# Kernel optimization log

Hardware: AMD Instinct MI355X
Metric: run time of the kernel (lower is better)

## Reference

```python
import jax, jax.numpy as jnp
import numpy as np

B, T, C, H = 4, 2048, 1024, 16
D = C // H


def setup_inputs() -> dict:
    key = jax.random.key(0)
    ks = jax.random.split(key, 6)
    s = 1.0 / np.sqrt(C)
    return {
        "x": jax.random.normal(ks[0], (B, T, C), dtype=jnp.float32),
        "attention_mask": jnp.ones((B, 1, T), dtype=jnp.int32),
        "Wq": jax.random.normal(ks[1], (C, C), dtype=jnp.float32) * s,
        "bq": jnp.zeros((C,), dtype=jnp.float32),
        "Wk": jax.random.normal(ks[2], (C, C), dtype=jnp.float32) * s,
        "bk": jnp.zeros((C,), dtype=jnp.float32),
        "Wv": jax.random.normal(ks[3], (C, C), dtype=jnp.float32) * s,
        "bv": jnp.zeros((C,), dtype=jnp.float32),
        "Wp": jax.random.normal(ks[4], (C, C), dtype=jnp.float32) * s,
        "bp": jnp.zeros((C,), dtype=jnp.float32),
    }


def reference(x, attention_mask, Wq, bq, Wk, bk, Wv, bv, Wp, bp):
    b, t, c = x.shape
    d = c // H
    # projections (torch Linear: x @ W^T + b)
    q = (x @ Wq.T + bq).reshape(b, t, H, d).transpose(0, 2, 1, 3)  # [B,H,T,D]
    k = (x @ Wk.T + bk).reshape(b, t, H, d).transpose(0, 2, 1, 3)
    v = (x @ Wv.T + bv).reshape(b, t, H, d).transpose(0, 2, 1, 3)
    attn = jnp.einsum("bhqd,bhkd->bhqk", q, k) / jnp.sqrt(jnp.asarray(d, x.dtype))
    mask = attention_mask[:, :, :t]  # [B,1,T] -> broadcast over [B,H,T,T] keys
    attn = jnp.where(mask[:, :, None, :] == 0, jnp.asarray(-jnp.inf, x.dtype), attn)
    attn = jax.nn.softmax(attn, axis=-1)  # dropout p=0 (eval)
    y = jnp.einsum("bhqk,bhkd->bhqd", attn, v)
    y = y.transpose(0, 2, 1, 3).reshape(b, t, c)
    return y @ Wp.T + bp
```

## Files before the change

### kernel.cpp

```cpp
#include <hip/hip_runtime.h>


#define TT 2048
#define CC 1024
#define HH 16
#define DD 64
#define BB 4

typedef unsigned short u16;
typedef unsigned int u32;
typedef __attribute__((ext_vector_type(8))) short bf16x8;
typedef __attribute__((ext_vector_type(4))) float f32x4;
typedef __attribute__((ext_vector_type(4))) u32 u32x4;

#if __has_builtin(__builtin_amdgcn_exp2f)
#define EXP2(x) __builtin_amdgcn_exp2f(x)
#else
#define EXP2(x) __expf((x) * 0.6931471805599453f)
#endif

__device__ __forceinline__ u16 f2bf(float f) {
    u32 u = __builtin_bit_cast(u32, f);
    u += 0x7FFFu + ((u >> 16) & 1u);
    return (u16)(u >> 16);
}
__device__ __forceinline__ u32 pk2(float a, float b) {
    u32 ua = __builtin_bit_cast(u32, a); ua += 0x7FFFu + ((ua >> 16) & 1u);
    u32 ub = __builtin_bit_cast(u32, b); ub += 0x7FFFu + ((ub >> 16) & 1u);
    return __builtin_amdgcn_perm(ub, ua, 0x07060302);
}
__device__ __forceinline__ u32 cvtpk(float lo, float hi) {
    u32 r;
    asm("v_cvt_pk_bf16_f32 %0, %1, %2" : "=v"(r) : "v"(lo), "v"(hi));
    return r;
}

#define GLDS(g, l) __builtin_amdgcn_global_load_lds( \
    (const __attribute__((address_space(1))) void*)(g), \
    (__attribute__((address_space(3))) void*)(l), 16, 0, 0)

__global__ __launch_bounds__(256) void wcvt(const float* __restrict__ s,
                                            u16* __restrict__ d, int n8) {
    const int i = blockIdx.x * 256 + threadIdx.x;
    if (i < n8) {
        const float4 f0 = ((const float4*)s)[2 * i];
        const float4 f1 = ((const float4*)s)[2 * i + 1];
        uint4 w;
        w.x = pk2(f0.x, f0.y); w.y = pk2(f0.z, f0.w);
        w.z = pk2(f1.x, f1.y); w.w = pk2(f1.z, f1.w);
        ((uint4*)d)[i] = w;
    }
}

__global__ __launch_bounds__(256) void wcvt3(const float* __restrict__ s0,
                                             const float* __restrict__ s1,
                                             const float* __restrict__ s2,
                                             u16* __restrict__ d0,
                                             u16* __restrict__ d1,
                                             u16* __restrict__ d2, int n8) {
    const int which = blockIdx.y;
    const float* s = (which == 0) ? s0 : (which == 1) ? s1 : s2;
    u16* d = (which == 0) ? d0 : (which == 1) ? d1 : d2;
    const int i = blockIdx.x * 256 + threadIdx.x;
    if (i < n8) {
        const float4 f0 = ((const float4*)s)[2 * i];
        const float4 f1 = ((const float4*)s)[2 * i + 1];
        uint4 w;
        w.x = pk2(f0.x, f0.y); w.y = pk2(f0.z, f0.w);
        w.z = pk2(f1.x, f1.y); w.w = pk2(f1.z, f1.w);
        ((uint4*)d)[i] = w;
    }
}

template <int PROJ>
__global__ __launch_bounds__(256) void gemmX(const u16* __restrict__ A,
                                             const u16* __restrict__ Wb,
                                             const float* __restrict__ b0,
                                             const float* __restrict__ b1,
                                             const float* __restrict__ b2,
                                             void* __restrict__ out0,
                                             void* __restrict__ out1,
                                             void* __restrict__ out2) {
    __shared__ u16 As[128 * 64];
    __shared__ u16 Bs[128 * 64];

    const int tid  = threadIdx.x;
    const int wave = tid >> 6, lane = tid & 63;
    const int quad = lane >> 4, l16 = lane & 15;
    const int bm = blockIdx.y * 128, bn = blockIdx.x * 128;
    const int wm = (wave >> 1) * 64, wn = (wave & 1) * 64;
    const int K = CC;

    f32x4 acc[4][4] = {};

    for (int k0 = 0; k0 < K; k0 += 64) {
#pragma unroll
        for (int rr = 0; rr < 4; rr++) {
            const int c = rr * 256 + tid;
            const int row = c >> 3;
            const int cs = ((c & 7) ^ (row & 7)) * 8;
            GLDS(&Wb[(size_t)(bn + row) * K + k0 + cs], &Bs[c * 8]);
        }
#pragma unroll
        for (int rr = 0; rr < 4; rr++) {
            const int c = rr * 256 + tid;
            const int row = c >> 3;
            const int cs = ((c & 7) ^ (row & 7)) * 8;
            GLDS(&A[(size_t)(bm + row) * K + k0 + cs], &As[c * 8]);
        }
        __syncthreads();

#pragma unroll
        for (int ks = 0; ks < 2; ks++) {
            bf16x8 af[4], bfr[4];
#pragma unroll
            for (int i = 0; i < 4; i++) {
                const int row = wm + i * 16 + l16;
                const int s8 = (ks * 4 + quad) ^ (row & 7);
                af[i] = *(bf16x8*)&As[row * 64 + s8 * 8];
            }
#pragma unroll
            for (int j = 0; j < 4; j++) {
                const int row = wn + j * 16 + l16;
                const int s8 = (ks * 4 + quad) ^ (row & 7);
                bfr[j] = *(bf16x8*)&Bs[row * 64 + s8 * 8];
            }
#pragma unroll
            for (int i = 0; i < 4; i++)
#pragma unroll
                for (int j = 0; j < 4; j++)
                    acc[i][j] = __builtin_amdgcn_mfma_f32_16x16x32_bf16(af[i], bfr[j], acc[i][j], 0, 0, 0);
        }
        __syncthreads();
    }

    if (PROJ) {
        float* out = (float*)out0;
#pragma unroll
        for (int j = 0; j < 4; j++) {
            const int col = bn + wn + j * 16 + l16;
            const float bv = b0[col];
#pragma unroll
            for (int i = 0; i < 4; i++) {
                const int row0 = bm + wm + i * 16 + quad * 4;
#pragma unroll
                for (int r = 0; r < 4; r++)
                    out[(size_t)(row0 + r) * CC + col] = acc[i][j][r] + bv;
            }
        }
    } else {
        const int mid = bn >> 10;
        const float* bias = (mid == 0) ? b0 : (mid == 1) ? b1 : b2;
#pragma unroll
        for (int j = 0; j < 4; j++) {
            const int col  = bn + wn + j * 16 + l16;
            const int colL = col & (CC - 1);
            const float bv = bias[colL];
#pragma unroll
            for (int i = 0; i < 4; i++) {
                const int row0 = bm + wm + i * 16 + quad * 4;
                if (mid < 2) {
                    u16* out = (u16*)(mid ? out1 : out0);
#pragma unroll
                    for (int r = 0; r < 4; r++)
                        out[(size_t)(row0 + r) * CC + colL] = f2bf(acc[i][j][r] + bv);
                } else {
                    const int hh = colL >> 6, dch = colL & 63;
                    const int bb = row0 >> 11, t0 = row0 & (TT - 1);
                    const size_t idx = (((size_t)bb * HH + hh) * DD + dch) * TT + t0;
                    uint2 w;
                    w.x = pk2(acc[i][j][0] + bv, acc[i][j][1] + bv);
                    w.y = pk2(acc[i][j][2] + bv, acc[i][j][3] + bv);
                    *(uint2*)&((u16*)out2)[idx] = w;
                }
            }
        }
    }
}

__global__ __launch_bounds__(512) void attn(const u16* __restrict__ Q,
                                            const u16* __restrict__ Kb,
                                            const u16* __restrict__ Vt,
                                            const int* __restrict__ mask,
                                            u16* __restrict__ Y) {
    const int b = blockIdx.z, h = blockIdx.y, qt = blockIdx.x;
    const int tid  = threadIdx.x;
    const int wave = tid >> 6, lane = tid & 63;
    const int quad = lane >> 4, l16 = lane & 15;
    const int qrow0 = qt * 256 + wave * 32;

    __shared__ u16 Ks[2][64 * 64];
    __shared__ u16 Vs[2][64 * 64];
    __shared__ __align__(16) float bias_lds[TT];

    const size_t qb = ((size_t)b * TT + qrow0) * CC + h * DD;

    bf16x8 qf[2][2];
#pragma unroll
    for (int m = 0; m < 2; m++)
#pragma unroll
        for (int ks = 0; ks < 2; ks++)
            qf[m][ks] = *(const bf16x8*)&Q[qb + (size_t)(m * 16 + l16) * CC + ks * 32 + quad * 8];

    {
        const int i = tid * 4;
        const int4 m0 = *(const int4*)&mask[b * TT + i];
        bias_lds[i + 0] = m0.x ? 0.f : -1e38f;
        bias_lds[i + 1] = m0.y ? 0.f : -1e38f;
        bias_lds[i + 2] = m0.z ? 0.f : -1e38f;
        bias_lds[i + 3] = m0.w ? 0.f : -1e38f;
    }

    const int c0 = tid;
    const int r0 = c0 >> 3;
    const int kp0 = (c0 & 7) ^ ((((r0 >> 3) & 1) << 2) | (r0 & 3));
    const int vp0 = (c0 & 7) ^ (r0 & 7);
    const u16* kgp = Kb + ((size_t)b * TT) * CC + h * DD;
    const u16* vgp = Vt + ((size_t)(b * HH + h) * DD) * TT;

    const int rowA = ((l16 >> 2) << 3) | (l16 & 3);
    const int s0k  = (((l16 >> 2) & 1) << 2) | (l16 & 3);

    f32x4 o[2][4] = {};
    float lsum[2] = {};
    const float SC = 0.18033688011112042f;

    GLDS(&kgp[(size_t)r0 * CC + kp0 * 8], &Ks[0][c0 * 8]);
    GLDS(&vgp[(size_t)r0 * TT + vp0 * 8], &Vs[0][c0 * 8]);
    asm volatile("s_waitcnt vmcnt(0) lgkmcnt(0)" ::: "memory");
    __builtin_amdgcn_s_barrier();
    __builtin_amdgcn_sched_barrier(0);

#pragma unroll 1
    for (int kt = 0; kt < TT; kt += 64) {
        const int cur = (kt >> 6) & 1;
        const u16* Kc = &Ks[cur][0];
        const u16* Vc = &Vs[cur][0];

        if (kt + 64 < TT) {
            const int nxt = cur ^ 1;
            GLDS(&kgp[(size_t)(kt + 64 + r0) * CC + kp0 * 8], &Ks[nxt][c0 * 8]);
            GLDS(&vgp[(size_t)r0 * TT + kt + 64 + vp0 * 8], &Vs[nxt][c0 * 8]);
        }

        const f32x4 bA = *(const f32x4*)&bias_lds[kt + quad * 8];
        const f32x4 bB = *(const f32x4*)&bias_lds[kt + quad * 8 + 4];
        const f32x4 bC = *(const f32x4*)&bias_lds[kt + 32 + quad * 8];
        const f32x4 bD = *(const f32x4*)&bias_lds[kt + 32 + quad * 8 + 4];

        f32x4 s2[2][4] = {};
        __builtin_amdgcn_s_setprio(1);
#pragma unroll
        for (int n = 0; n < 4; n++) {
            const int rowK = rowA + (n & 1) * 4 + (n >> 1) * 32;
#pragma unroll
            for (int ks = 0; ks < 2; ks++) {
                const int pos = ((ks << 2) + quad) ^ s0k;
                const bf16x8 kf = *(const bf16x8*)&Kc[rowK * 64 + pos * 8];
#pragma unroll
                for (int m = 0; m < 2; m++)
                    s2[m][n] = __builtin_amdgcn_mfma_f32_16x16x32_bf16(kf, qf[m][ks], s2[m][n], 0, 0, 0);
            }
        }
        __builtin_amdgcn_s_setprio(0);

#pragma unroll
        for (int ks = 0; ks < 2; ks++) {
            bf16x8 pf[2];
#pragma unroll
            for (int m = 0; m < 2; m++) {
                u32 pw[4];
#pragma unroll
                for (int nn = 0; nn < 2; nn++) {
                    const int n = 2 * ks + nn;
                    const f32x4 bv = (n == 0) ? bA : (n == 1) ? bB : (n == 2) ? bC : bD;
                    const float p0 = EXP2(fmaf(s2[m][n][0], SC, bv[0]));
                    const float p1 = EXP2(fmaf(s2[m][n][1], SC, bv[1]));
                    const float p2 = EXP2(fmaf(s2[m][n][2], SC, bv[2]));
                    const float p3 = EXP2(fmaf(s2[m][n][3], SC, bv[3]));
                    lsum[m] += (p0 + p1) + (p2 + p3);
                    pw[2 * nn]     = cvtpk(p0, p1);
                    pw[2 * nn + 1] = cvtpk(p2, p3);
                }
                const u32x4 t = { pw[0], pw[1], pw[2], pw[3] };
                pf[m] = __builtin_bit_cast(bf16x8, t);
            }
            __builtin_amdgcn_s_setprio(1);
#pragma unroll
            for (int dt = 0; dt < 4; dt++) {
                const int vrow = dt * 16 + l16;
                const int pos = ((ks << 2) + quad) ^ (vrow & 7);
                const bf16x8 vf = *(const bf16x8*)&Vc[vrow * 64 + pos * 8];
#pragma unroll
                for (int m = 0; m < 2; m++)
                    o[m][dt] = __builtin_amdgcn_mfma_f32_16x16x32_bf16(pf[m], vf, o[m][dt], 0, 0, 0);
            }
            __builtin_amdgcn_s_setprio(0);
        }

        asm volatile("s_waitcnt vmcnt(0)" ::: "memory");
        __builtin_amdgcn_sched_barrier(0);
        __builtin_amdgcn_s_barrier();
    }

#pragma unroll
    for (int m = 0; m < 2; m++) {
        lsum[m] += __shfl_xor(lsum[m], 16, 64);
        lsum[m] += __shfl_xor(lsum[m], 32, 64);
    }

#pragma unroll
    for (int m = 0; m < 2; m++) {
        float inv[4];
#pragma unroll
        for (int r = 0; r < 4; r++)
            inv[r] = 1.0f / __shfl(lsum[m], quad * 4 + r, 64);
#pragma unroll
        for (int dt = 0; dt < 4; dt++)
#pragma unroll
            for (int r = 0; r < 4; r++)
                Y[qb + (size_t)(m * 16 + quad * 4 + r) * CC + dt * 16 + l16] = f2bf(o[m][dt][r] * inv[r]);
    }
}

extern "C" void kernel_launch(void* const* d_in, const int* in_sizes, int n_in,
                              void* d_out, int out_size, void* d_ws, size_t ws_size,
                              hipStream_t stream) {
    const float* x    = (const float*)d_in[0];
    const int*   mask = (const int*)d_in[1];
    const float* Wq   = (const float*)d_in[2];
    const float* bq   = (const float*)d_in[3];
    const float* Wk   = (const float*)d_in[4];
    const float* bk   = (const float*)d_in[5];
    const float* Wv   = (const float*)d_in[6];
    const float* bv   = (const float*)d_in[7];
    const float* Wp   = (const float*)d_in[8];
    const float* bp   = (const float*)d_in[9];

    u16* ws = (u16*)d_ws;
    const size_t sz = (size_t)BB * TT * CC;
    u16* Qb   = ws;
    u16* Kbuf = ws + sz;
    u16* Vtb  = ws + 2 * sz;

    u16* xb   = (u16*)d_out;
    u16* Wq16 = xb + sz;
    u16* Wk16 = Wq16 + (size_t)CC * CC;
    u16* Wv16 = Wk16 + (size_t)CC * CC;

    const int W8 = CC * CC / 8;
    wcvt<<<4096, 256, 0, stream>>>(x, xb, (int)(sz / 8));
    wcvt3<<<dim3(512, 3), 256, 0, stream>>>(Wq, Wk, Wv, Wq16, Wk16, Wv16, W8);

    gemmX<0><<<dim3(24, 64), 256, 0, stream>>>(xb, Wq16, bq, bk, bv, Qb, Kbuf, Vtb);

    attn<<<dim3(TT / 256, HH, BB), 512, 0, stream>>>(Qb, Kbuf, Vtb, mask, Qb);

    wcvt<<<512, 256, 0, stream>>>(Wp, Kbuf, W8);
    gemmX<1><<<dim3(8, 64), 256, 0, stream>>>(Qb, Kbuf, bp, nullptr, nullptr, d_out, nullptr, nullptr);
}
```

Measured before the change: 289.5 us.

## Use 256x256 double-buffered QKV GEMM, merge conversions, fuse Wp cast into projection

Replaces the 128x128 QKV projection GEMM with a 256x256-tile, 512-thread kernel. It double-buffers LDS through async global-to-LDS loads, swizzles block order for L2 locality and raises wave priority around the MFMA section. The x and QKV-weight conversion kernels are merged into one launch, and the Wp fp32-to-bf16 conversion is folded into the output projection's tile loading, dropping a separate kernel. The trade-offs are 128KB of dynamic LDS with fewer resident blocks, and in the output GEMM synchronous fp32 loads plus conversion in the inner loop.

```diff
diff --git a/kernel.cpp b/kernel.cpp
--- a/kernel.cpp
+++ b/kernel.cpp
@@ -39,48 +39,147 @@
     (const __attribute__((address_space(1))) void*)(g), \
     (__attribute__((address_space(3))) void*)(l), 16, 0, 0)
 
-__global__ __launch_bounds__(256) void wcvt(const float* __restrict__ s,
-                                            u16* __restrict__ d, int n8) {
-    const int i = blockIdx.x * 256 + threadIdx.x;
-    if (i < n8) {
-        const float4 f0 = ((const float4*)s)[2 * i];
-        const float4 f1 = ((const float4*)s)[2 * i + 1];
-        uint4 w;
-        w.x = pk2(f0.x, f0.y); w.y = pk2(f0.z, f0.w);
-        w.z = pk2(f1.x, f1.y); w.w = pk2(f1.z, f1.w);
-        ((uint4*)d)[i] = w;
-    }
-}
-
-__global__ __launch_bounds__(256) void wcvt3(const float* __restrict__ s0,
-                                             const float* __restrict__ s1,
-                                             const float* __restrict__ s2,
-                                             u16* __restrict__ d0,
-                                             u16* __restrict__ d1,
-                                             u16* __restrict__ d2, int n8) {
-    const int which = blockIdx.y;
-    const float* s = (which == 0) ? s0 : (which == 1) ? s1 : s2;
-    u16* d = (which == 0) ? d0 : (which == 1) ? d1 : d2;
-    const int i = blockIdx.x * 256 + threadIdx.x;
-    if (i < n8) {
-        const float4 f0 = ((const float4*)s)[2 * i];
-        const float4 f1 = ((const float4*)s)[2 * i + 1];
-        uint4 w;
-        w.x = pk2(f0.x, f0.y); w.y = pk2(f0.z, f0.w);
-        w.z = pk2(f1.x, f1.y); w.w = pk2(f1.z, f1.w);
-        ((uint4*)d)[i] = w;
-    }
-}
-
-template <int PROJ>
-__global__ __launch_bounds__(256) void gemmX(const u16* __restrict__ A,
-                                             const u16* __restrict__ Wb,
+__global__ __launch_bounds__(256) void wcvtA(const float* __restrict__ x,
+                                             const float* __restrict__ Wq,
+                                             const float* __restrict__ Wk,
+                                             const float* __restrict__ Wv,
+                                             u16* __restrict__ xb,
+                                             u16* __restrict__ Wq16,
+                                             u16* __restrict__ Wk16,
+                                             u16* __restrict__ Wv16) {
+    const int bid = blockIdx.x;
+    const float* s; u16* d; int i;
+    if (bid < 4096) {
+        s = x; d = xb; i = bid * 256 + threadIdx.x;
+    } else {
+        const int t = bid - 4096;
+        const int which = t >> 9, sub = t & 511;
+        s = (which == 0) ? Wq : (which == 1) ? Wk : Wv;
+        d = (which == 0) ? Wq16 : (which == 1) ? Wk16 : Wv16;
+        i = sub * 256 + threadIdx.x;
+    }
+    const float4 f0 = ((const float4*)s)[2 * i];
+    const float4 f1 = ((const float4*)s)[2 * i + 1];
+    uint4 w;
+    w.x = pk2(f0.x, f0.y); w.y = pk2(f0.z, f0.w);
+    w.z = pk2(f1.x, f1.y); w.w = pk2(f1.z, f1.w);
+    ((uint4*)d)[i] = w;
+}
+
+__global__ __launch_bounds__(512, 2) void gemm256(const u16* __restrict__ A,
+                                                  const u16* __restrict__ Wb,
+                                                  const float* __restrict__ b0,
+                                                  const float* __restrict__ b1,
+                                                  const float* __restrict__ b2,
+                                                  u16* __restrict__ outQ,
+                                                  u16* __restrict__ outK,
+                                                  u16* __restrict__ outV) {
+    extern __shared__ u16 lds[];
+    const int tid  = threadIdx.x;
+    const int wave = tid >> 6, lane = tid & 63;
+    const int quad = lane >> 4, l16 = lane & 15;
+    const int wr = wave >> 2, wc = wave & 3;
+
+    const int bid0 = blockIdx.y * 12 + blockIdx.x;
+    const int bid  = (bid0 & 7) * 48 + (bid0 >> 3);
+    const int bn = (bid % 12) * 256, bm = (bid / 12) * 256;
+    const int K = CC;
+
+    u16* const As0 = lds;
+    u16* const Bs0 = lds + 32768;
+
+    int rows[4], css[4];
+#pragma unroll
+    for (int g = 0; g < 4; g++) {
+        const int c = g * 512 + tid;
+        rows[g] = c >> 3;
+        css[g]  = ((c & 7) ^ ((c >> 3) & 7)) * 8;
+    }
+
+    f32x4 acc[8][4] = {};
+
+    auto STAGE = [&](int buf, int k0) {
+#pragma unroll
+        for (int g = 0; g < 4; g++)
+            GLDS(&A[(size_t)(bm + rows[g]) * K + k0 + css[g]],
+                 &As0[buf * 16384 + (g * 512 + tid) * 8]);
+#pragma unroll
+        for (int g = 0; g < 4; g++)
+            GLDS(&Wb[(size_t)(bn + rows[g]) * K + k0 + css[g]],
+                 &Bs0[buf * 16384 + (g * 512 + tid) * 8]);
+    };
+
+    STAGE(0, 0);
+    asm volatile("s_waitcnt vmcnt(0)" ::: "memory");
+    __builtin_amdgcn_s_barrier();
+    __builtin_amdgcn_sched_barrier(0);
+
+#pragma unroll 1
+    for (int t = 0; t < 16; t++) {
+        const int buf = t & 1;
+        if (t < 15) STAGE(buf ^ 1, (t + 1) * 64);
+
+        const u16* Ab = &As0[buf * 16384];
+        const u16* Bb = &Bs0[buf * 16384];
+        __builtin_amdgcn_s_setprio(1);
+#pragma unroll
+        for (int ks = 0; ks < 2; ks++) {
+            bf16x8 bfr[4];
+#pragma unroll
+            for (int j = 0; j < 4; j++) {
+                const int rb = wc * 64 + j * 16 + l16;
+                const int p = ((ks << 2) + quad) ^ (rb & 7);
+                bfr[j] = *(const bf16x8*)&Bb[rb * 64 + p * 8];
+            }
+#pragma unroll
+            for (int i = 0; i < 8; i++) {
+                const int ra = wr * 128 + i * 16 + l16;
+                const int p = ((ks << 2) + quad) ^ (ra & 7);
+                const bf16x8 af = *(const bf16x8*)&Ab[ra * 64 + p * 8];
+#pragma unroll
+                for (int j = 0; j < 4; j++)
+                    acc[i][j] = __builtin_amdgcn_mfma_f32_16x16x32_bf16(af, bfr[j], acc[i][j], 0, 0, 0);
+            }
+        }
+        __builtin_amdgcn_s_setprio(0);
+
+        asm volatile("s_waitcnt vmcnt(0)" ::: "memory");
+        __builtin_amdgcn_sched_barrier(0);
+        __builtin_amdgcn_s_barrier();
+    }
+
+    const int mid = bn >> 10;
+    const float* bias = (mid == 0) ? b0 : (mid == 1) ? b1 : b2;
+#pragma unroll
+    for (int j = 0; j < 4; j++) {
+        const int col  = bn + wc * 64 + j * 16 + l16;
+        const int colL = col & (CC - 1);
+        const float bv = bias[colL];
+#pragma unroll
+        for (int i = 0; i < 8; i++) {
+            const int row0 = bm + wr * 128 + i * 16 + quad * 4;
+            if (mid < 2) {
+                u16* out = mid ? outK : outQ;
+#pragma unroll
+                for (int r = 0; r < 4; r++)
+                    out[(size_t)(row0 + r) * CC + colL] = f2bf(acc[i][j][r] + bv);
+            } else {
+                const int hh = colL >> 6, dch = colL & 63;
+                const int bb = row0 >> 11, t0 = row0 & (TT - 1);
+                const size_t idx = (((size_t)bb * HH + hh) * DD + dch) * TT + t0;
+                uint2 w;
+                w.x = pk2(acc[i][j][0] + bv, acc[i][j][1] + bv);
+                w.y = pk2(acc[i][j][2] + bv, acc[i][j][3] + bv);
+                *(uint2*)&outV[idx] = w;
+            }
+        }
+    }
+}
+
+__global__ __launch_bounds__(256) void gemmP(const u16* __restrict__ A,
+                                             const float* __restrict__ Wf,
                                              const float* __restrict__ b0,
-                                             const float* __restrict__ b1,
-                                             const float* __restrict__ b2,
-                                             void* __restrict__ out0,
-                                             void* __restrict__ out1,
-                                             void* __restrict__ out2) {
+                                             float* __restrict__ out) {
     __shared__ u16 As[128 * 64];
     __shared__ u16 Bs[128 * 64];
 
@@ -99,7 +198,12 @@
             const int c = rr * 256 + tid;
             const int row = c >> 3;
             const int cs = ((c & 7) ^ (row & 7)) * 8;
-            GLDS(&Wb[(size_t)(bn + row) * K + k0 + cs], &Bs[c * 8]);
+            const float4 f0 = *(const float4*)&Wf[(size_t)(bn + row) * K + k0 + cs];
+            const float4 f1 = *(const float4*)&Wf[(size_t)(bn + row) * K + k0 + cs + 4];
+            uint4 w;
+            w.x = pk2(f0.x, f0.y); w.y = pk2(f0.z, f0.w);
+            w.z = pk2(f1.x, f1.y); w.w = pk2(f1.z, f1.w);
+            *(uint4*)&Bs[c * 8] = w;
         }
 #pragma unroll
         for (int rr = 0; rr < 4; rr++) {
@@ -134,46 +238,16 @@
         __syncthreads();
     }
 
-    if (PROJ) {
-        float* out = (float*)out0;
-#pragma unroll
-        for (int j = 0; j < 4; j++) {
-            const int col = bn + wn + j * 16 + l16;
-            const float bv = b0[col];
-#pragma unroll
-            for (int i = 0; i < 4; i++) {
-                const int row0 = bm + wm + i * 16 + quad * 4;
-#pragma unroll
-                for (int r = 0; r < 4; r++)
-                    out[(size_t)(row0 + r) * CC + col] = acc[i][j][r] + bv;
-            }
-        }
-    } else {
-        const int mid = bn >> 10;
-        const float* bias = (mid == 0) ? b0 : (mid == 1) ? b1 : b2;
-#pragma unroll
-        for (int j = 0; j < 4; j++) {
-            const int col  = bn + wn + j * 16 + l16;
-            const int colL = col & (CC - 1);
-            const float bv = bias[colL];
-#pragma unroll
-            for (int i = 0; i < 4; i++) {
-                const int row0 = bm + wm + i * 16 + quad * 4;
-                if (mid < 2) {
-                    u16* out = (u16*)(mid ? out1 : out0);
-#pragma unroll
-                    for (int r = 0; r < 4; r++)
-                        out[(size_t)(row0 + r) * CC + colL] = f2bf(acc[i][j][r] + bv);
-                } else {
-                    const int hh = colL >> 6, dch = colL & 63;
-                    const int bb = row0 >> 11, t0 = row0 & (TT - 1);
-                    const size_t idx = (((size_t)bb * HH + hh) * DD + dch) * TT + t0;
-                    uint2 w;
-                    w.x = pk2(acc[i][j][0] + bv, acc[i][j][1] + bv);
-                    w.y = pk2(acc[i][j][2] + bv, acc[i][j][3] + bv);
-                    *(uint2*)&((u16*)out2)[idx] = w;
-                }
-            }
+#pragma unroll
+    for (int j = 0; j < 4; j++) {
+        const int col = bn + wn + j * 16 + l16;
+        const float bv = b0[col];
+#pragma unroll
+        for (int i = 0; i < 4; i++) {
+            const int row0 = bm + wm + i * 16 + quad * 4;
+#pragma unroll
+            for (int r = 0; r < 4; r++)
+                out[(size_t)(row0 + r) * CC + col] = acc[i][j][r] + bv;
         }
     }
 }
@@ -348,14 +422,18 @@
     u16* Wk16 = Wq16 + (size_t)CC * CC;
     u16* Wv16 = Wk16 + (size_t)CC * CC;
 
-    const int W8 = CC * CC / 8;
-    wcvt<<<4096, 256, 0, stream>>>(x, xb, (int)(sz / 8));
-    wcvt3<<<dim3(512, 3), 256, 0, stream>>>(Wq, Wk, Wv, Wq16, Wk16, Wv16, W8);
-
-    gemmX<0><<<dim3(24, 64), 256, 0, stream>>>(xb, Wq16, bq, bk, bv, Qb, Kbuf, Vtb);
+    static bool inited = false;
+    if (!inited) {
+        (void)hipFuncSetAttribute((const void*)gemm256,
+                                  hipFuncAttributeMaxDynamicSharedMemorySize, 131072);
+        inited = true;
+    }
+
+    wcvtA<<<5632, 256, 0, stream>>>(x, Wq, Wk, Wv, xb, Wq16, Wk16, Wv16);
+
+    gemm256<<<dim3(12, 32), 512, 131072, stream>>>(xb, Wq16, bq, bk, bv, Qb, Kbuf, Vtb);
 
     attn<<<dim3(TT / 256, HH, BB), 512, 0, stream>>>(Qb, Kbuf, Vtb, mask, Qb);
 
-    wcvt<<<512, 256, 0, stream>>>(Wp, Kbuf, W8);
-    gemmX<1><<<dim3(8, 64), 256, 0, stream>>>(Qb, Kbuf, bp, nullptr, nullptr, d_out, nullptr, nullptr);
-}
+    gemmP<<<dim3(8, 64), 256, 0, stream>>>(Qb, Wp, bp, (float*)d_out);
+}
```

New measurement: 288.9 us. Within noise of the previous version (-0.2%).

## Rewrite projection GEMMs with 4-stage LDS pipeline, larger tiles, and block swizzle

Applied to the files above, without the earlier changes.

Replaces the 128x128 single-buffered GEMM with a templated 256xBN tile kernel using 512 threads and a 4-deep ring of K=32 LDS stages. Global-to-LDS loads are issued three stages ahead and gated by explicit vmcnt waits, with one barrier per step. It also adds a block-index remap for L2 locality, MFMA priority hints, and merges the x and weight conversion kernels into one launch. The aim is to hide load latency and cut barrier stalls, at the cost of heavy dynamic LDS use (128KB/96KB), which lowers occupancy.

```diff
diff --git a/kernel.cpp b/kernel.cpp
--- a/kernel.cpp
+++ b/kernel.cpp
@@ -52,115 +52,191 @@
     }
 }
 
-__global__ __launch_bounds__(256) void wcvt3(const float* __restrict__ s0,
-                                             const float* __restrict__ s1,
-                                             const float* __restrict__ s2,
-                                             u16* __restrict__ d0,
-                                             u16* __restrict__ d1,
-                                             u16* __restrict__ d2, int n8) {
-    const int which = blockIdx.y;
-    const float* s = (which == 0) ? s0 : (which == 1) ? s1 : s2;
-    u16* d = (which == 0) ? d0 : (which == 1) ? d1 : d2;
-    const int i = blockIdx.x * 256 + threadIdx.x;
-    if (i < n8) {
-        const float4 f0 = ((const float4*)s)[2 * i];
-        const float4 f1 = ((const float4*)s)[2 * i + 1];
-        uint4 w;
-        w.x = pk2(f0.x, f0.y); w.y = pk2(f0.z, f0.w);
-        w.z = pk2(f1.x, f1.y); w.w = pk2(f1.z, f1.w);
-        ((uint4*)d)[i] = w;
-    }
-}
-
-template <int PROJ>
-__global__ __launch_bounds__(256) void gemmX(const u16* __restrict__ A,
-                                             const u16* __restrict__ Wb,
-                                             const float* __restrict__ b0,
-                                             const float* __restrict__ b1,
-                                             const float* __restrict__ b2,
-                                             void* __restrict__ out0,
-                                             void* __restrict__ out1,
-                                             void* __restrict__ out2) {
-    __shared__ u16 As[128 * 64];
-    __shared__ u16 Bs[128 * 64];
-
+__global__ __launch_bounds__(256) void wcvtA(const float* __restrict__ x,
+                                             const float* __restrict__ Wq,
+                                             const float* __restrict__ Wk,
+                                             const float* __restrict__ Wv,
+                                             u16* __restrict__ xb,
+                                             u16* __restrict__ Wq16,
+                                             u16* __restrict__ Wk16,
+                                             u16* __restrict__ Wv16) {
+    const int bid = blockIdx.x;
+    const float* s; u16* d; int i;
+    if (bid < 4096) {
+        s = x; d = xb; i = bid * 256 + threadIdx.x;
+    } else {
+        const int t = bid - 4096;
+        const int which = t >> 9, sub = t & 511;
+        s = (which == 0) ? Wq : (which == 1) ? Wk : Wv;
+        d = (which == 0) ? Wq16 : (which == 1) ? Wk16 : Wv16;
+        i = sub * 256 + threadIdx.x;
+    }
+    const float4 f0 = ((const float4*)s)[2 * i];
+    const float4 f1 = ((const float4*)s)[2 * i + 1];
+    uint4 w;
+    w.x = pk2(f0.x, f0.y); w.y = pk2(f0.z, f0.w);
+    w.z = pk2(f1.x, f1.y); w.w = pk2(f1.z, f1.w);
+    ((uint4*)d)[i] = w;
+}
+
+template <int BN, int WM, int WN, int MODE>
+__global__ __launch_bounds__(512, 2) void gemmT(const u16* __restrict__ Ag,
+                                                const u16* __restrict__ Bg,
+                                                const float* __restrict__ b0,
+                                                const float* __restrict__ b1,
+                                                const float* __restrict__ b2,
+                                                u16* __restrict__ outQ,
+                                                u16* __restrict__ outK,
+                                                u16* __restrict__ outV,
+                                                float* __restrict__ outF) {
+    constexpr int NI = WM / 16, NJ = WN / 16;
+    constexpr int WAVES_N = BN / WN;
+    constexpr int BUFSZ = (256 + BN) * 32;
+    constexpr int SPT = 2 + BN / 128;
+    constexpr int NT = CC / 32;
+
+    extern __shared__ u16 lds[];
     const int tid  = threadIdx.x;
     const int wave = tid >> 6, lane = tid & 63;
     const int quad = lane >> 4, l16 = lane & 15;
-    const int bm = blockIdx.y * 128, bn = blockIdx.x * 128;
-    const int wm = (wave >> 1) * 64, wn = (wave & 1) * 64;
-    const int K = CC;
-
-    f32x4 acc[4][4] = {};
-
-    for (int k0 = 0; k0 < K; k0 += 64) {
-#pragma unroll
-        for (int rr = 0; rr < 4; rr++) {
-            const int c = rr * 256 + tid;
-            const int row = c >> 3;
-            const int cs = ((c & 7) ^ (row & 7)) * 8;
-            GLDS(&Wb[(size_t)(bn + row) * K + k0 + cs], &Bs[c * 8]);
-        }
-#pragma unroll
-        for (int rr = 0; rr < 4; rr++) {
-            const int c = rr * 256 + tid;
-            const int row = c >> 3;
-            const int cs = ((c & 7) ^ (row & 7)) * 8;
-            GLDS(&A[(size_t)(bm + row) * K + k0 + cs], &As[c * 8]);
-        }
-        __syncthreads();
-
-#pragma unroll
-        for (int ks = 0; ks < 2; ks++) {
-            bf16x8 af[4], bfr[4];
-#pragma unroll
-            for (int i = 0; i < 4; i++) {
-                const int row = wm + i * 16 + l16;
-                const int s8 = (ks * 4 + quad) ^ (row & 7);
-                af[i] = *(bf16x8*)&As[row * 64 + s8 * 8];
-            }
-#pragma unroll
-            for (int j = 0; j < 4; j++) {
-                const int row = wn + j * 16 + l16;
-                const int s8 = (ks * 4 + quad) ^ (row & 7);
-                bfr[j] = *(bf16x8*)&Bs[row * 64 + s8 * 8];
-            }
-#pragma unroll
-            for (int i = 0; i < 4; i++)
-#pragma unroll
-                for (int j = 0; j < 4; j++)
-                    acc[i][j] = __builtin_amdgcn_mfma_f32_16x16x32_bf16(af[i], bfr[j], acc[i][j], 0, 0, 0);
-        }
-        __syncthreads();
-    }
-
-    if (PROJ) {
-        float* out = (float*)out0;
-#pragma unroll
-        for (int j = 0; j < 4; j++) {
-            const int col = bn + wn + j * 16 + l16;
+    const int wr = wave / WAVES_N, wc = wave & (WAVES_N - 1);
+
+    const int NBX = (BN == 256) ? 12 : 8;
+    const int bid0 = blockIdx.y * NBX + blockIdx.x;
+    const int chunk = (NBX * 32) >> 3;
+    const int bid  = (bid0 & 7) * chunk + (bid0 >> 3);
+    const int bn = (bid % NBX) * BN, bm = (bid / NBX) * 256;
+
+    size_t aOff[2]; int aDst[2];
+#pragma unroll
+    for (int g = 0; g < 2; g++) {
+        const int c = g * 512 + tid;
+        const int row = c >> 2;
+        const int kc = (c & 3) ^ ((row >> 1) & 3);
+        aOff[g] = (size_t)(bm + row) * CC + kc * 8;
+        aDst[g] = c * 8;
+    }
+    size_t bOff[BN / 128]; int bDst[BN / 128];
+#pragma unroll
+    for (int g = 0; g < BN / 128; g++) {
+        const int c = g * 512 + tid;
+        const int row = c >> 2;
+        const int kc = (c & 3) ^ ((row >> 1) & 3);
+        bOff[g] = (size_t)(bn + row) * CC + kc * 8;
+        bDst[g] = 8192 + c * 8;
+    }
+
+    int aRd[NI], bRd[NJ];
+#pragma unroll
+    for (int i = 0; i < NI; i++) {
+        const int row = wr * WM + i * 16 + l16;
+        const int p = quad ^ ((row >> 1) & 3);
+        aRd[i] = row * 32 + p * 8;
+    }
+#pragma unroll
+    for (int j = 0; j < NJ; j++) {
+        const int row = wc * WN + j * 16 + l16;
+        const int p = quad ^ ((row >> 1) & 3);
+        bRd[j] = 8192 + row * 32 + p * 8;
+    }
+
+    f32x4 acc[NI][NJ] = {};
+
+#define STAGE_T(t)                                                        \
+    {                                                                     \
+        u16* dst = &lds[((t) & 3) * BUFSZ];                               \
+        const int k0 = (t) * 32;                                          \
+        _Pragma("unroll")                                                 \
+        for (int g = 0; g < 2; g++)                                       \
+            GLDS(&Ag[aOff[g] + k0], &dst[aDst[g]]);                       \
+        _Pragma("unroll")                                                 \
+        for (int g = 0; g < BN / 128; g++)                                \
+            GLDS(&Bg[bOff[g] + k0], &dst[bDst[g]]);                       \
+    }
+
+#define COMPUTE_T(t)                                                      \
+    {                                                                     \
+        const u16* buf = &lds[((t) & 3) * BUFSZ];                         \
+        bf16x8 af[NI], bfr[NJ];                                           \
+        _Pragma("unroll")                                                 \
+        for (int i = 0; i < NI; i++) af[i] = *(const bf16x8*)&buf[aRd[i]];\
+        _Pragma("unroll")                                                 \
+        for (int j = 0; j < NJ; j++) bfr[j] = *(const bf16x8*)&buf[bRd[j]];\
+        __builtin_amdgcn_s_setprio(1);                                    \
+        _Pragma("unroll")                                                 \
+        for (int i = 0; i < NI; i++)                                      \
+            _Pragma("unroll")                                             \
+            for (int j = 0; j < NJ; j++)                                  \
+                acc[i][j] = __builtin_amdgcn_mfma_f32_16x16x32_bf16(      \
+                    af[i], bfr[j], acc[i][j], 0, 0, 0);                   \
+        __builtin_amdgcn_s_setprio(0);                                    \
+    }
+
+#define WAIT_MAIN()                                                       \
+    if constexpr (SPT == 4) asm volatile("s_waitcnt vmcnt(8)" ::: "memory"); \
+    else                    asm volatile("s_waitcnt vmcnt(6)" ::: "memory");
+#define WAIT_ONE()                                                        \
+    if constexpr (SPT == 4) asm volatile("s_waitcnt vmcnt(4)" ::: "memory"); \
+    else                    asm volatile("s_waitcnt vmcnt(3)" ::: "memory");
+
+    STAGE_T(0); STAGE_T(1); STAGE_T(2);
+    WAIT_MAIN();
+    __builtin_amdgcn_sched_barrier(0);
+    __builtin_amdgcn_s_barrier();
+    __builtin_amdgcn_sched_barrier(0);
+
+#pragma unroll 1
+    for (int t = 0; t < NT - 3; t++) {
+        STAGE_T(t + 3);
+        COMPUTE_T(t);
+        WAIT_MAIN();
+        __builtin_amdgcn_sched_barrier(0);
+        __builtin_amdgcn_s_barrier();
+        __builtin_amdgcn_sched_barrier(0);
+    }
+    COMPUTE_T(NT - 3);
+    WAIT_ONE();
+    __builtin_amdgcn_sched_barrier(0);
+    __builtin_amdgcn_s_barrier();
+    __builtin_amdgcn_sched_barrier(0);
+    COMPUTE_T(NT - 2);
+    asm volatile("s_waitcnt vmcnt(0)" ::: "memory");
+    __builtin_amdgcn_sched_barrier(0);
+    __builtin_amdgcn_s_barrier();
+    __builtin_amdgcn_sched_barrier(0);
+    COMPUTE_T(NT - 1);
+
+#undef STAGE_T
+#undef COMPUTE_T
+#undef WAIT_MAIN
+#undef WAIT_ONE
+
+    if (MODE == 1) {
+#pragma unroll
+        for (int j = 0; j < NJ; j++) {
+            const int col = bn + wc * WN + j * 16 + l16;
             const float bv = b0[col];
 #pragma unroll
-            for (int i = 0; i < 4; i++) {
-                const int row0 = bm + wm + i * 16 + quad * 4;
+            for (int i = 0; i < NI; i++) {
+                const int row0 = bm + wr * WM + i * 16 + quad * 4;
 #pragma unroll
                 for (int r = 0; r < 4; r++)
-                    out[(size_t)(row0 + r) * CC + col] = acc[i][j][r] + bv;
+                    outF[(size_t)(row0 + r) * CC + col] = acc[i][j][r] + bv;
             }
         }
     } else {
         const int mid = bn >> 10;
         const float* bias = (mid == 0) ? b0 : (mid == 1) ? b1 : b2;
 #pragma unroll
-        for (int j = 0; j < 4; j++) {
-            const int col  = bn + wn + j * 16 + l16;
+        for (int j = 0; j < NJ; j++) {
+            const int col  = bn + wc * WN + j * 16 + l16;
             const int colL = col & (CC - 1);
             const float bv = bias[colL];
 #pragma unroll
-            for (int i = 0; i < 4; i++) {
-                const int row0 = bm + wm + i * 16 + quad * 4;
+            for (int i = 0; i < NI; i++) {
+                const int row0 = bm + wr * WM + i * 16 + quad * 4;
                 if (mid < 2) {
-                    u16* out = (u16*)(mid ? out1 : out0);
+                    u16* out = mid ? outK : outQ;
 #pragma unroll
                     for (int r = 0; r < 4; r++)
                         out[(size_t)(row0 + r) * CC + colL] = f2bf(acc[i][j][r] + bv);
@@ -171,7 +247,7 @@
                     uint2 w;
                     w.x = pk2(acc[i][j][0] + bv, acc[i][j][1] + bv);
                     w.y = pk2(acc[i][j][2] + bv, acc[i][j][3] + bv);
-                    *(uint2*)&((u16*)out2)[idx] = w;
+                    *(uint2*)&outV[idx] = w;
                 }
             }
         }
@@ -348,14 +424,26 @@
     u16* Wk16 = Wq16 + (size_t)CC * CC;
     u16* Wv16 = Wk16 + (size_t)CC * CC;
 
+    static bool inited = false;
+    if (!inited) {
+        (void)hipFuncSetAttribute((const void*)gemmT<256, 128, 64, 0>,
+                                  hipFuncAttributeMaxDynamicSharedMemorySize, 131072);
+        (void)hipFuncSetAttribute((const void*)gemmT<128, 64, 64, 1>,
+                                  hipFuncAttributeMaxDynamicSharedMemorySize, 98304);
+        inited = true;
+    }
+
     const int W8 = CC * CC / 8;
-    wcvt<<<4096, 256, 0, stream>>>(x, xb, (int)(sz / 8));
-    wcvt3<<<dim3(512, 3), 256, 0, stream>>>(Wq, Wk, Wv, Wq16, Wk16, Wv16, W8);
-
-    gemmX<0><<<dim3(24, 64), 256, 0, stream>>>(xb, Wq16, bq, bk, bv, Qb, Kbuf, Vtb);
+
+    wcvtA<<<5632, 256, 0, stream>>>(x, Wq, Wk, Wv, xb, Wq16, Wk16, Wv16);
+
+    gemmT<256, 128, 64, 0><<<dim3(12, 32), 512, 131072, stream>>>(
+        xb, Wq16, bq, bk, bv, Qb, Kbuf, Vtb, nullptr);
 
     attn<<<dim3(TT / 256, HH, BB), 512, 0, stream>>>(Qb, Kbuf, Vtb, mask, Qb);
 
     wcvt<<<512, 256, 0, stream>>>(Wp, Kbuf, W8);
-    gemmX<1><<<dim3(8, 64), 256, 0, stream>>>(Qb, Kbuf, bp, nullptr, nullptr, d_out, nullptr, nullptr);
-}
+
+    gemmT<128, 64, 64, 1><<<dim3(8, 32), 512, 98304, stream>>>(
+        Qb, Kbuf, bp, nullptr, nullptr, nullptr, nullptr, nullptr, (float*)d_out);
+}
```

After: 279.1 us. -3.6%, faster.
